# Kernel tuning notes

Measured on AMD Instinct MI355X. Metric: run time of the kernel, lower is better.

The kernel has to match this reference:

```python
import jax, jax.numpy as jnp
import numpy as np

B, L, D, H = 2, 2048, 1024, 16
HD = D // H  # head_dim = 64


def setup_inputs() -> dict:
    key = jax.random.key(0)
    k1, k2, k3 = jax.random.split(key, 3)
    x = jax.random.normal(k1, (B, L, D), dtype=jnp.float32)
    # nn.Linear(d_model, 3*d_model): weight [3D, D], bias [3D]
    lim = 1.0 / np.sqrt(D)
    W_qkv = jax.random.uniform(k2, (3 * D, D), dtype=jnp.float32, minval=-lim, maxval=lim)
    b_qkv = jax.random.uniform(k3, (3 * D,), dtype=jnp.float32, minval=-lim, maxval=lim)
    return {"x": x, "W_qkv": W_qkv, "b_qkv": b_qkv}


def reference(x, W_qkv, b_qkv):
    b, l, d = x.shape
    qkv = x @ W_qkv.T + b_qkv                      # [b, l, 3d]
    q, k, v = jnp.split(qkv, 3, axis=-1)           # each [b, l, d]
    # split heads: [b, l, h, hd]
    q = q.reshape(b, l, H, HD)
    k = k.reshape(b, l, H, HD)
    v = v.reshape(b, l, H, HD)
    scale = 1.0 / np.sqrt(HD).astype(np.float32)
    # scores [b, h, l, l]
    scores = jnp.einsum('bqhd,bkhd->bhqk', q, k) * scale
    attn = jax.nn.softmax(scores, axis=-1)
    out = jnp.einsum('bhqk,bkhd->bqhd', attn, v)   # [b, l, h, hd]
    return out.reshape(b, l, d)
```

## Files before the change

kernel.cpp:

```cpp
#include <hip/hip_runtime.h>

#define BATCH 2
#define SEQ 2048
#define DMODEL 1024
#define NH 16
#define HD 64
#define M_TOT (BATCH*SEQ)
#define N_TOT (3*DMODEL)
#define K_TOT (DMODEL)
#define NQK   (2*DMODEL)
#define QSCALE 0.18033688011112042f

typedef __attribute__((ext_vector_type(8)))  _Float16 f16x8;
typedef __attribute__((ext_vector_type(4)))  float    f32x4;
typedef __attribute__((ext_vector_type(16))) float    f32x16;

static __device__ __forceinline__ unsigned short f2h(float f) {
  _Float16 h = (_Float16)f;
  return __builtin_bit_cast(unsigned short, h);
}

static __device__ __forceinline__ f32x16 zero16() {
  f32x16 z;
  #pragma unroll
  for (int i = 0; i < 16; ++i) z[i] = 0.f;
  return z;
}

static __device__ __forceinline__ void async16(const unsigned short* g, unsigned short* l) {
  __builtin_amdgcn_global_load_lds(
      (const __attribute__((address_space(1))) unsigned*)g,
      (__attribute__((address_space(3))) unsigned*)l, 16, 0, 0);
}

static __device__ __forceinline__ void barrier_f() {
  asm volatile("" ::: "memory");
  __builtin_amdgcn_s_barrier();
  asm volatile("" ::: "memory");
}

__global__ __launch_bounds__(256) void cast_f16_2(
    const float* __restrict__ xsrc, const float* __restrict__ wsrc,
    unsigned short* __restrict__ xdst, unsigned short* __restrict__ wdst,
    int n8x, int n8tot)
{
  int i = blockIdx.x * 256 + threadIdx.x;
  if (i >= n8tot) return;
  const float* src;
  unsigned short* dst;
  int idx;
  if (i < n8x) { src = xsrc; dst = xdst; idx = i; }
  else         { src = wsrc; dst = wdst; idx = i - n8x; }
  float4 v0 = ((const float4*)src)[2*idx];
  float4 v1 = ((const float4*)src)[2*idx + 1];
  uint4 pk;
  pk.x = (unsigned)f2h(v0.x) | ((unsigned)f2h(v0.y) << 16);
  pk.y = (unsigned)f2h(v0.z) | ((unsigned)f2h(v0.w) << 16);
  pk.z = (unsigned)f2h(v1.x) | ((unsigned)f2h(v1.y) << 16);
  pk.w = (unsigned)f2h(v1.z) | ((unsigned)f2h(v1.w) << 16);
  ((uint4*)dst)[idx] = pk;
}

__global__ __launch_bounds__(256) void qkv_gemm_mfma(
    const unsigned short* __restrict__ Xh,
    const unsigned short* __restrict__ Wh,
    const float* __restrict__ bias,
    unsigned short* __restrict__ QK,
    unsigned short* __restrict__ VT)
{
  __shared__ unsigned short As[128][32];
  __shared__ unsigned short Bs[128][32];

  const int tid  = threadIdx.x;
  const int wave = tid >> 6;
  const int lane = tid & 63;
  const int l15  = lane & 15;
  const int quad = lane >> 4;

  const int lin = blockIdx.x + blockIdx.y * 24;
  const int c   = lin & 7;
  const int w   = lin >> 3;
  const int bxl = (c & 1) * 12 + (w % 12);
  const int byl = (c >> 1) * 8 + (w / 12);

  const bool isV = (bxl >= (NQK/128));
  const int n0 = (isV ? (bxl - NQK/128) : bxl) * 128;
  const int m0 = byl * 128;

  const unsigned short* Arows = isV ? (Wh + (size_t)(NQK + n0) * K_TOT)
                                    : (Xh + (size_t)m0 * K_TOT);
  const unsigned short* Brows = isV ? (Xh + (size_t)m0 * K_TOT)
                                    : (Wh + (size_t)n0 * K_TOT);

  const int srow = tid >> 2;
  const int skc  = (tid & 3) * 8;
  const unsigned short* Ag0 = Arows + (size_t)srow * K_TOT + skc;
  const unsigned short* Ag1 = Arows + (size_t)(64 + srow) * K_TOT + skc;
  const unsigned short* Bg0 = Brows + (size_t)srow * K_TOT + skc;
  const unsigned short* Bg1 = Brows + (size_t)(64 + srow) * K_TOT + skc;
  unsigned short* Al = &As[0][0] + tid * 8;
  unsigned short* Bl = &Bs[0][0] + tid * 8;

  const int wm = (wave & 1) * 64;
  const int wn = (wave >> 1) * 64;

  f32x4 acc[4][4];
  #pragma unroll
  for (int i = 0; i < 4; ++i)
    #pragma unroll
    for (int j = 0; j < 4; ++j) acc[i][j] = (f32x4){0.f,0.f,0.f,0.f};

  for (int k0 = 0; k0 < K_TOT; k0 += 32) {
    __syncthreads();
    async16(Ag0 + k0, Al);
    async16(Ag1 + k0, Al + 2048);
    async16(Bg0 + k0, Bl);
    async16(Bg1 + k0, Bl + 2048);
    __syncthreads();

    f16x8 af[4], bf[4];
    #pragma unroll
    for (int i = 0; i < 4; ++i)
      af[i] = *(const f16x8*)&As[wm + i*16 + l15][quad*8];
    #pragma unroll
    for (int j = 0; j < 4; ++j)
      bf[j] = *(const f16x8*)&Bs[wn + j*16 + l15][quad*8];
    #pragma unroll
    for (int i = 0; i < 4; ++i)
      #pragma unroll
      for (int j = 0; j < 4; ++j)
        acc[i][j] = __builtin_amdgcn_mfma_f32_16x16x32_f16(af[i], bf[j], acc[i][j], 0, 0, 0);
  }

  if (!isV) {
    const float sc = (n0 < DMODEL) ? QSCALE : 1.0f;
    float bv[4];
    #pragma unroll
    for (int j = 0; j < 4; ++j) bv[j] = bias[n0 + wn + j*16 + l15];
    #pragma unroll
    for (int i = 0; i < 4; ++i)
      #pragma unroll
      for (int j = 0; j < 4; ++j)
        #pragma unroll
        for (int r = 0; r < 4; ++r) {
          const size_t row = (size_t)(m0 + wm + i*16 + quad*4 + r);
          QK[row * NQK + n0 + wn + j*16 + l15] = f2h((acc[i][j][r] + bv[j]) * sc);
        }
  } else {
    const int bidx  = m0 >> 11;
    const int sbase = (m0 & 2047) + wn;
    #pragma unroll
    for (int i = 0; i < 4; ++i)
      #pragma unroll
      for (int r = 0; r < 4; ++r) {
        const int nn = n0 + wm + i*16 + quad*4 + r;
        const float bb = bias[NQK + nn];
        unsigned short* drow =
            VT + ((size_t)(bidx*NH + (nn >> 6)) * HD + (nn & 63)) * SEQ + sbase;
        #pragma unroll
        for (int j = 0; j < 4; ++j)
          drow[j*16 + l15] = f2h(acc[i][j][r] + bb);
      }
  }
}

__global__ __launch_bounds__(256) void attn_mfma3(
    const unsigned short* __restrict__ QK,
    const unsigned short* __restrict__ VT,
    float* __restrict__ out)
{
  __shared__ unsigned short Ks[2][64][64];
  __shared__ unsigned short Vs[2][64][64];
  __shared__ unsigned short Ps[4][32][72];
  __shared__ float Dn[4][32];

  const int tid  = threadIdx.x;
  const int wv   = tid >> 6;
  const int lane = tid & 63;
  const int l31  = lane & 31;
  const int h32  = lane >> 5;
  const int qsw  = l31 >> 3;

  const int lin = blockIdx.x + ((blockIdx.y + (blockIdx.z << 4)) << 4);
  const int logical = ((lin & 7) << 6) + (lin >> 3);
  const int qt   = logical & 15;
  const int head = logical >> 4;
  const int hh   = head & 15;
  const int b    = head >> 4;
  const int q0 = qt*128 + wv*32;

  f16x8 qf[4];
  {
    const unsigned short* qrow = QK + (size_t)(b*SEQ + q0 + l31) * NQK + hh*HD;
    #pragma unroll
    for (int f = 0; f < 4; ++f)
      qf[f] = *(const f16x8*)(qrow + f*16 + h32*8);
  }

  const unsigned short* Kg = QK + (size_t)b*SEQ*NQK + DMODEL + hh*HD;
  const unsigned short* Vg = VT + (size_t)(b*NH + hh) * HD * SEQ;

  const int sr = tid >> 3;
  const int sp = tid & 7;
  const int sg = ((sp - sr) & 7) * 8;

  const unsigned short* kg0 = Kg + (size_t)sr      * NQK + sg;
  const unsigned short* kg1 = Kg + (size_t)(sr+32) * NQK + sg;
  const unsigned short* vg0 = Vg + (size_t)sr      * SEQ + sg;
  const unsigned short* vg1 = Vg + (size_t)(sr+32) * SEQ + sg;
  unsigned short* kl = &Ks[0][0][0] + tid*8;
  unsigned short* vl = &Vs[0][0][0] + tid*8;

  f32x16 oacc[2];
  oacc[0] = zero16();
  oacc[1] = zero16();
  float dsv[4] = {0.f, 0.f, 0.f, 0.f};

  auto STAGE = [&](int kt, int bb) {
    const size_t krow = (size_t)kt * 64 * NQK;
    const int    kcol = kt * 64;
    async16(kg0 + krow, kl + bb*4096);
    async16(kg1 + krow, kl + bb*4096 + 2048);
    async16(vg0 + kcol, vl + bb*4096);
    async16(vg1 + kcol, vl + bb*4096 + 2048);
  };

  auto COMPUTE = [&](int bb) {
    const unsigned short* ks = &Ks[bb][0][0];
    const unsigned short* vs = &Vs[bb][0][0];

    f32x16 sa[2];
    sa[0] = zero16();
    sa[1] = zero16();
    __builtin_amdgcn_s_setprio(1);
    #pragma unroll
    for (int f = 0; f < 4; ++f) {
      const int g = f*2 + h32;
      #pragma unroll
      for (int kb = 0; kb < 2; ++kb) {
        const int row = kb*32 + l31;
        f16x8 kf = *(const f16x8*)(ks + row*64 + ((g + row) & 7) * 8);
        sa[kb] = __builtin_amdgcn_mfma_f32_32x32x16_f16(kf, qf[f], sa[kb], 0, 0, 0);
      }
    }
    __builtin_amdgcn_s_setprio(0);

    #pragma unroll
    for (int kb = 0; kb < 2; ++kb) {
      #pragma unroll
      for (int g4 = 0; g4 < 4; ++g4) {
        unsigned short hsv[4];
        #pragma unroll
        for (int r = 0; r < 4; ++r) {
          float p = exp2f(sa[kb][g4*4 + r]);
          dsv[r] += p;
          hsv[r] = f2h(p);
        }
        unsigned short* dst =
            &Ps[wv][l31][(((kb*4 + g4) ^ qsw) & 7) * 8 + h32*4];
        uint2 pk;
        pk.x = (unsigned)hsv[0] | ((unsigned)hsv[1] << 16);
        pk.y = (unsigned)hsv[2] | ((unsigned)hsv[3] << 16);
        *(uint2*)dst = pk;
      }
    }

    __builtin_amdgcn_s_setprio(1);
    #pragma unroll
    for (int f = 0; f < 4; ++f) {
      const int g = f*2 + h32;
      f16x8 pf = *(const f16x8*)&Ps[wv][l31][((g ^ qsw) & 7) * 8];
      #pragma unroll
      for (int jd = 0; jd < 2; ++jd) {
        const int row = jd*32 + l31;
        f16x8 vf = *(const f16x8*)(vs + row*64 + ((g + row) & 7) * 8);
        oacc[jd] = __builtin_amdgcn_mfma_f32_32x32x16_f16(pf, vf, oacc[jd], 0, 0, 0);
      }
    }
    __builtin_amdgcn_s_setprio(0);
  };

  #define A_STEP(kt, sb, cb) \
    STAGE((kt)+1, (sb)); \
    asm volatile("s_waitcnt vmcnt(4)" ::: "memory"); \
    barrier_f(); \
    COMPUTE((cb)); \
    barrier_f();

  STAGE(0, 0);
  for (int kt = 0; kt < 30; kt += 2) {
    A_STEP(kt,   1, 0)
    A_STEP(kt+1, 0, 1)
  }
  A_STEP(30, 1, 0)
  asm volatile("s_waitcnt vmcnt(0)" ::: "memory");
  barrier_f();
  COMPUTE(1);
  #undef A_STEP

  float dsum = (dsv[0] + dsv[1]) + (dsv[2] + dsv[3]);
  dsum += __shfl_xor(dsum, 32, 64);
  Dn[wv][l31] = 1.f / dsum;

  #pragma unroll
  for (int jd = 0; jd < 2; ++jd) {
    #pragma unroll
    for (int g4 = 0; g4 < 4; ++g4) {
      #pragma unroll
      for (int r = 0; r < 4; ++r) {
        const int qrow = g4*8 + h32*4 + r;
        const float oval = oacc[jd][g4*4 + r] * Dn[wv][qrow];
        out[(size_t)(b*SEQ + q0 + qrow) * DMODEL + hh*HD + jd*32 + l31] = oval;
      }
    }
  }
}

extern "C" void kernel_launch(void* const* d_in, const int* in_sizes, int n_in,
                              void* d_out, int out_size, void* d_ws, size_t ws_size,
                              hipStream_t stream) {
  const float* x    = (const float*)d_in[0];
  const float* W    = (const float*)d_in[1];
  const float* bias = (const float*)d_in[2];
  float* out = (float*)d_out;

  unsigned short* qk = (unsigned short*)d_ws;
  unsigned short* vt = qk + (size_t)M_TOT * NQK;
  unsigned short* xh = vt + (size_t)BATCH * NH * HD * SEQ;
  unsigned short* wh = xh + (size_t)M_TOT * K_TOT;

  const int n8x = M_TOT*K_TOT/8;
  const int n8w = N_TOT*K_TOT/8;
  cast_f16_2<<<(n8x + n8w + 255)/256, 256, 0, stream>>>(x, W, xh, wh, n8x, n8x + n8w);

  dim3 g1(N_TOT/128, M_TOT/128);
  qkv_gemm_mfma<<<g1, 256, 0, stream>>>(xh, wh, bias, qk, vt);

  dim3 g2(SEQ/128, NH, BATCH);
  attn_mfma3<<<g2, 256, 0, stream>>>(qk, vt, out);
}
```

Measured before the change: 174.3 us.

## Split KV range across wave pairs in 512-thread attention blocks

The attention kernel moves to 512 threads (8 waves). Each pair of waves shares a 32-row query slice, and each wave of the pair processes alternate 64-key tiles. The two partial outputs and softmax denominators are merged through LDS before the final normalized store. The double-buffered async prefetch pipeline is replaced by a simple load-barrier-compute loop that loads two tiles per step, which gives more waves for latency hiding but drops the overlap of loads with compute and adds a cross-wave reduction.

```diff
diff --git a/kernel.cpp b/kernel.cpp
--- a/kernel.cpp
+++ b/kernel.cpp
@@ -31,12 +31,6 @@
   __builtin_amdgcn_global_load_lds(
       (const __attribute__((address_space(1))) unsigned*)g,
       (__attribute__((address_space(3))) unsigned*)l, 16, 0, 0);
-}
-
-static __device__ __forceinline__ void barrier_f() {
-  asm volatile("" ::: "memory");
-  __builtin_amdgcn_s_barrier();
-  asm volatile("" ::: "memory");
 }
 
 __global__ __launch_bounds__(256) void cast_f16_2(
@@ -164,18 +158,18 @@
   }
 }
 
-__global__ __launch_bounds__(256) void attn_mfma3(
+__global__ __launch_bounds__(512) void attn_mfma3(
     const unsigned short* __restrict__ QK,
     const unsigned short* __restrict__ VT,
     float* __restrict__ out)
 {
-  __shared__ unsigned short Ks[2][64][64];
-  __shared__ unsigned short Vs[2][64][64];
-  __shared__ unsigned short Ps[4][32][72];
-  __shared__ float Dn[4][32];
+  __shared__ unsigned short SM[4*4096];
+  __shared__ unsigned short Ps[8][32][72];
+  __shared__ float Dn[8][32];
 
   const int tid  = threadIdx.x;
   const int wv   = tid >> 6;
+  const int par  = wv & 1;
   const int lane = tid & 63;
   const int l31  = lane & 31;
   const int h32  = lane >> 5;
@@ -187,7 +181,7 @@
   const int head = logical >> 4;
   const int hh   = head & 15;
   const int b    = head >> 4;
-  const int q0 = qt*128 + wv*32;
+  const int q0 = qt*128 + (wv >> 1)*32;
 
   f16x8 qf[4];
   {
@@ -203,31 +197,24 @@
   const int sr = tid >> 3;
   const int sp = tid & 7;
   const int sg = ((sp - sr) & 7) * 8;
-
-  const unsigned short* kg0 = Kg + (size_t)sr      * NQK + sg;
-  const unsigned short* kg1 = Kg + (size_t)(sr+32) * NQK + sg;
-  const unsigned short* vg0 = Vg + (size_t)sr      * SEQ + sg;
-  const unsigned short* vg1 = Vg + (size_t)(sr+32) * SEQ + sg;
-  unsigned short* kl = &Ks[0][0][0] + tid*8;
-  unsigned short* vl = &Vs[0][0][0] + tid*8;
+  const unsigned short* kgB = Kg + (size_t)sr * NQK + sg;
+  const unsigned short* vgB = Vg + (size_t)sr * SEQ + sg;
+
+  const unsigned short* ks = SM + par*4096;
+  const unsigned short* vs = SM + 8192 + par*4096;
 
   f32x16 oacc[2];
   oacc[0] = zero16();
   oacc[1] = zero16();
   float dsv[4] = {0.f, 0.f, 0.f, 0.f};
 
-  auto STAGE = [&](int kt, int bb) {
-    const size_t krow = (size_t)kt * 64 * NQK;
-    const int    kcol = kt * 64;
-    async16(kg0 + krow, kl + bb*4096);
-    async16(kg1 + krow, kl + bb*4096 + 2048);
-    async16(vg0 + kcol, vl + bb*4096);
-    async16(vg1 + kcol, vl + bb*4096 + 2048);
-  };
-
-  auto COMPUTE = [&](int bb) {
-    const unsigned short* ks = &Ks[bb][0][0];
-    const unsigned short* vs = &Vs[bb][0][0];
+  for (int p = 0; p < 16; ++p) {
+    __syncthreads();
+    async16(kgB + (size_t)(2*p  )*64*NQK, SM         + tid*8);
+    async16(kgB + (size_t)(2*p+1)*64*NQK, SM +  4096 + tid*8);
+    async16(vgB + (2*p  )*64,             SM +  8192 + tid*8);
+    async16(vgB + (2*p+1)*64,             SM + 12288 + tid*8);
+    __syncthreads();
 
     f32x16 sa[2];
     sa[0] = zero16();
@@ -252,9 +239,9 @@
         unsigned short hsv[4];
         #pragma unroll
         for (int r = 0; r < 4; ++r) {
-          float p = exp2f(sa[kb][g4*4 + r]);
-          dsv[r] += p;
-          hsv[r] = f2h(p);
+          float ppv = exp2f(sa[kb][g4*4 + r]);
+          dsv[r] += ppv;
+          hsv[r] = f2h(ppv);
         }
         unsigned short* dst =
             &Ps[wv][l31][(((kb*4 + g4) ^ qsw) & 7) * 8 + h32*4];
@@ -278,39 +265,43 @@
       }
     }
     __builtin_amdgcn_s_setprio(0);
-  };
-
-  #define A_STEP(kt, sb, cb) \
-    STAGE((kt)+1, (sb)); \
-    asm volatile("s_waitcnt vmcnt(4)" ::: "memory"); \
-    barrier_f(); \
-    COMPUTE((cb)); \
-    barrier_f();
-
-  STAGE(0, 0);
-  for (int kt = 0; kt < 30; kt += 2) {
-    A_STEP(kt,   1, 0)
-    A_STEP(kt+1, 0, 1)
-  }
-  A_STEP(30, 1, 0)
-  asm volatile("s_waitcnt vmcnt(0)" ::: "memory");
-  barrier_f();
-  COMPUTE(1);
-  #undef A_STEP
+  }
 
   float dsum = (dsv[0] + dsv[1]) + (dsv[2] + dsv[3]);
   dsum += __shfl_xor(dsum, 32, 64);
-  Dn[wv][l31] = 1.f / dsum;
-
-  #pragma unroll
-  for (int jd = 0; jd < 2; ++jd) {
-    #pragma unroll
-    for (int g4 = 0; g4 < 4; ++g4) {
-      #pragma unroll
-      for (int r = 0; r < 4; ++r) {
-        const int qrow = g4*8 + h32*4 + r;
-        const float oval = oacc[jd][g4*4 + r] * Dn[wv][qrow];
-        out[(size_t)(b*SEQ + q0 + qrow) * DMODEL + hh*HD + jd*32 + l31] = oval;
+
+  __syncthreads();
+  float* xb = (float*)(&Ps[0][0][0]);
+  if (par) {
+    float* dst = xb + ((size_t)(wv >> 1) * 64 + lane) * 33;
+    #pragma unroll
+    for (int jd = 0; jd < 2; ++jd)
+      #pragma unroll
+      for (int i = 0; i < 16; ++i)
+        dst[jd*16 + i] = oacc[jd][i];
+    Dn[wv][l31] = dsum;
+  }
+  __syncthreads();
+  if (!par) {
+    const float* src = xb + ((size_t)(wv >> 1) * 64 + lane) * 33;
+    #pragma unroll
+    for (int jd = 0; jd < 2; ++jd)
+      #pragma unroll
+      for (int i = 0; i < 16; ++i)
+        oacc[jd][i] += src[jd*16 + i];
+    const float dtot = dsum + Dn[wv + 1][l31];
+    Dn[wv][l31] = 1.f / dtot;
+
+    #pragma unroll
+    for (int jd = 0; jd < 2; ++jd) {
+      #pragma unroll
+      for (int g4 = 0; g4 < 4; ++g4) {
+        #pragma unroll
+        for (int r = 0; r < 4; ++r) {
+          const int qrow = g4*8 + h32*4 + r;
+          const float oval = oacc[jd][g4*4 + r] * Dn[wv][qrow];
+          out[(size_t)(b*SEQ + q0 + qrow) * DMODEL + hh*HD + jd*32 + l31] = oval;
+        }
       }
     }
   }
@@ -337,5 +328,5 @@
   qkv_gemm_mfma<<<g1, 256, 0, stream>>>(xh, wh, bias, qk, vt);
 
   dim3 g2(SEQ/128, NH, BATCH);
-  attn_mfma3<<<g2, 256, 0, stream>>>(qk, vt, out);
-}
+  attn_mfma3<<<g2, 512, 0, stream>>>(qk, vt, out);
+}
```

Result: faster. 170.4 us (-2.2%).
